# Kernel tuning notes

Measured on AMD Instinct MI355X. Metric: run time of the kernel, lower is better.

The kernel has to match this reference:

```python
import jax, jax.numpy as jnp
import numpy as np

# PDELayer config (matches torch defaults)
Nx, Ny = 48, 48
Lx, Ly = 1.0, 1.0
T, dt = 0.01, 0.001
dx, dy = Lx / Nx, Ly / Ny
Nt = int(T / dt)  # 10 sequential stencil steps
B = 16384


def setup_inputs() -> dict:
    key = jax.random.key(0)
    u0 = jax.random.normal(key, (B, 1, Nx, Ny), dtype=jnp.float32)
    alpha_w = jnp.array([0.1, 0.1, 0.1], dtype=jnp.float32)  # alpha_w1..3
    beta_w = jnp.array([0.3, 0.2, 0.2], dtype=jnp.float32)   # beta_w1..3
    return {"u0": u0, "alpha_w": alpha_w, "beta_w": beta_w}


def _coeff_grids(alpha_w, beta_w):
    x = jnp.linspace(0.0, Lx, Nx, dtype=jnp.float32)
    y = jnp.linspace(0.0, Ly, Ny, dtype=jnp.float32)
    yy, xx = jnp.meshgrid(y, x, indexing='ij')  # [Ny, Nx]
    two_pi = jnp.float32(2.0 * np.pi)
    alpha_grid = 0.5 * dt * (alpha_w[0]
                             + alpha_w[1] * jnp.sin(two_pi * yy)
                             + alpha_w[2] * jnp.sin(2.0 * two_pi * yy)) / dx ** 2
    beta_grid = dt * (beta_w[0]
                      + beta_w[1] * jnp.cos(two_pi * xx)
                      + beta_w[2] * jnp.cos(2.0 * two_pi * xx)) / dy ** 2
    return alpha_grid[None], beta_grid[None]  # [1, Nx, Ny] (Nx==Ny)


def reference(u0, alpha_w, beta_w):
    alpha_grid, beta_grid = _coeff_grids(alpha_w, beta_w)
    # reflect-pad once; boundary ring stays frozen during time stepping
    u = jnp.pad(u0[:, 0], ((0, 0), (1, 1), (1, 1)), mode='reflect')  # [B, Nx+2, Ny+2]

    def step(u, _):
        ui = u[:, 1:-1, 1:-1]
        u_xx = u[:, 2:, 1:-1] - 2.0 * ui + u[:, :-2, 1:-1]
        u_yy = u[:, 1:-1, 2:] - 2.0 * ui + u[:, 1:-1, :-2]
        u = u.at[:, 1:-1, 1:-1].set(ui + alpha_grid * u_xx + beta_grid * u_yy)
        return u, None

    u, _ = jax.lax.scan(step, u, None, length=Nt)
    return u[:, 1:-1, 1:-1][:, None]  # [B, 1, Nx, Ny]
```

## Files before the change

kernel.cpp:

```cpp
#include <hip/hip_runtime.h>


typedef float v2f __attribute__((ext_vector_type(2)));

constexpr int NXY   = 48;
constexpr int CELLS = NXY * NXY;
constexpr int NT    = 10;
constexpr int WPB   = 4;
constexpr int TPB   = 64 * WPB;

__device__ __forceinline__ float dpp_up(float oldv, float src) {
    return __int_as_float(__builtin_amdgcn_update_dpp(
        __float_as_int(oldv), __float_as_int(src), 0x111, 0xF, 0xF, false));
}
__device__ __forceinline__ float dpp_dn(float oldv, float src) {
    return __int_as_float(__builtin_amdgcn_update_dpp(
        __float_as_int(oldv), __float_as_int(src), 0x101, 0xF, 0xF, false));
}
__device__ __forceinline__ v2f dpp_up2(v2f o, v2f s) {
    v2f r; r.x = dpp_up(o.x, s.x); r.y = dpp_up(o.y, s.y); return r;
}
__device__ __forceinline__ v2f dpp_dn2(v2f o, v2f s) {
    v2f r; r.x = dpp_dn(o.x, s.x); r.y = dpp_dn(o.y, s.y); return r;
}

__global__ __launch_bounds__(TPB)
__attribute__((amdgpu_waves_per_eu(4, 8)))
void pde_heat_kernel(
    const float* __restrict__ u0,
    const float* __restrict__ aw,
    const float* __restrict__ bw,
    float* __restrict__ out)
{
    const int lane = threadIdx.x & 63;
    const int img  = blockIdx.x * WPB + (threadIdx.x >> 6);
    const int r = lane & 15;
    const int c = lane >> 4;
    const float4* __restrict__ u4 = (const float4*)(u0 + (long long)img * CELLS);
    float4*       __restrict__ o4 = (float4*)(out + (long long)img * CELLS);

    const int fb = r * 36 + c * 3;

    v2f v[3][6];
    #pragma unroll
    for (int ii = 0; ii < 3; ++ii)
        #pragma unroll
        for (int k = 0; k < 3; ++k) {
            float4 t = u4[fb + 12 * ii + k];
            v[ii][2*k]   = (v2f){t.x, t.y};
            v[ii][2*k+1] = (v2f){t.z, t.w};
        }

    const float a0 = aw[0], a1 = aw[1], a2 = aw[2];
    const float b0 = bw[0], b1 = bw[1], b2 = bw[2];
    float ca[3];
    #pragma unroll
    for (int ii = 0; ii < 3; ++ii) {
        float y = (float)(3 * r + ii) * (1.0f / 47.0f);
        ca[ii] = 1.152f * (a0 + a1 * __builtin_amdgcn_sinf(y)
                              + a2 * __builtin_amdgcn_sinf(2.0f * y));
    }
    v2f cb2[6];
    #pragma unroll
    for (int k = 0; k < 6; ++k) {
        float x0 = (float)(12 * c + 2 * k)     * (1.0f / 47.0f);
        float x1 = (float)(12 * c + 2 * k + 1) * (1.0f / 47.0f);
        cb2[k].x = 2.304f * (b0 + b1 * __builtin_amdgcn_cosf(x0)
                                + b2 * __builtin_amdgcn_cosf(2.0f * x0));
        cb2[k].y = 2.304f * (b0 + b1 * __builtin_amdgcn_cosf(x1)
                                + b2 * __builtin_amdgcn_cosf(2.0f * x1));
    }

    v2f gV[6];
    #pragma unroll
    for (int k = 0; k < 6; ++k) gV[k] = v[1][k];
    float gH[3];
    #pragma unroll
    for (int ii = 0; ii < 3; ++ii) gH[ii] = (c == 0) ? v[ii][0].y : v[ii][5].x;

    const int laneL = lane - 16, laneR = lane + 16;

    for (int t = 0; t < NT; ++t) {
        v2f hb[6], above[6];
        #pragma unroll
        for (int k = 0; k < 6; ++k) hb[k]    = dpp_dn2(gV[k], v[0][k]);
        #pragma unroll
        for (int k = 0; k < 6; ++k) above[k] = dpp_up2(gV[k], v[2][k]);

        #pragma unroll
        for (int ii = 0; ii < 3; ++ii) {
            float hl = __shfl(v[ii][5].y, laneL);
            float hr = __shfl(v[ii][0].x, laneR);
            hl = (c == 0) ? gH[ii] : hl;
            hr = (c == 3) ? gH[ii] : hr;

            v2f L[6], R[6];
            L[0] = (v2f){hl, v[ii][0].x};
            #pragma unroll
            for (int k = 1; k < 6; ++k) L[k] = (v2f){v[ii][k-1].y, v[ii][k].x};
            #pragma unroll
            for (int k = 0; k < 5; ++k) R[k] = (v2f){v[ii][k].y, v[ii][k+1].x};
            R[5] = (v2f){v[ii][5].y, hr};

            v2f nrow[6];
            #pragma unroll
            for (int k = 0; k < 6; ++k) {
                v2f cv    = v[ii][k];
                v2f below = (ii < 2) ? v[ii + 1][k] : hb[k];
                v2f uxx = (above[k] + below) - 2.0f * cv;
                v2f uyy = (L[k] + R[k])      - 2.0f * cv;
                nrow[k] = cv + ca[ii] * uxx + cb2[k] * uyy;
            }
            #pragma unroll
            for (int k = 0; k < 6; ++k) {
                above[k] = v[ii][k];
                v[ii][k] = nrow[k];
            }
        }
    }

    #pragma unroll
    for (int ii = 0; ii < 3; ++ii)
        #pragma unroll
        for (int k = 0; k < 3; ++k) {
            float4 t;
            t.x = v[ii][2*k].x;   t.y = v[ii][2*k].y;
            t.z = v[ii][2*k+1].x; t.w = v[ii][2*k+1].y;
            o4[fb + 12 * ii + k] = t;
        }
}

extern "C" void kernel_launch(void* const* d_in, const int* in_sizes, int n_in,
                              void* d_out, int out_size, void* d_ws, size_t ws_size,
                              hipStream_t stream) {
    const float* u0 = (const float*)d_in[0];
    const float* aw = (const float*)d_in[1];
    const float* bw = (const float*)d_in[2];
    float* out = (float*)d_out;

    const int B = in_sizes[0] / CELLS;
    pde_heat_kernel<<<B / WPB, TPB, 0, stream>>>(u0, aw, bw, out);
}
```

Measured before the change: 89.83 us.

## Pack two images per wavefront with six-row tiles per lane

Each wave now processes two 48x48 images, one per 32-lane half. Each lane holds a 6x12 tile instead of 3x12, which halves the thread count and the halo exchanges per cell. Vertical halos use bound-ctrl DPP row shifts with boundary selects, the time loop is fully unrolled, and the update is written as explicit fmas with per-column coefficients. The waves-per-EU hint drops to 2–4 to leave room for the larger register footprint, at the cost of less latency hiding for the global loads and stores.

```diff
diff --git a/kernel.cpp b/kernel.cpp
--- a/kernel.cpp
+++ b/kernel.cpp
@@ -9,124 +9,113 @@
 constexpr int WPB   = 4;
 constexpr int TPB   = 64 * WPB;
 
-__device__ __forceinline__ float dpp_up(float oldv, float src) {
+__device__ __forceinline__ float dpp_shr1(float x) {
     return __int_as_float(__builtin_amdgcn_update_dpp(
-        __float_as_int(oldv), __float_as_int(src), 0x111, 0xF, 0xF, false));
+        0, __float_as_int(x), 0x111, 0xF, 0xF, true));
 }
-__device__ __forceinline__ float dpp_dn(float oldv, float src) {
+__device__ __forceinline__ float dpp_shl1(float x) {
     return __int_as_float(__builtin_amdgcn_update_dpp(
-        __float_as_int(oldv), __float_as_int(src), 0x101, 0xF, 0xF, false));
-}
-__device__ __forceinline__ v2f dpp_up2(v2f o, v2f s) {
-    v2f r; r.x = dpp_up(o.x, s.x); r.y = dpp_up(o.y, s.y); return r;
-}
-__device__ __forceinline__ v2f dpp_dn2(v2f o, v2f s) {
-    v2f r; r.x = dpp_dn(o.x, s.x); r.y = dpp_dn(o.y, s.y); return r;
+        0, __float_as_int(x), 0x101, 0xF, 0xF, true));
 }
 
 __global__ __launch_bounds__(TPB)
-__attribute__((amdgpu_waves_per_eu(4, 8)))
-void pde_heat_kernel(
-    const float* __restrict__ u0,
-    const float* __restrict__ aw,
-    const float* __restrict__ bw,
-    float* __restrict__ out)
+__attribute__((amdgpu_waves_per_eu(2, 4)))
+void pde_heat_kernel(const float* __restrict__ u0,
+                     const float* __restrict__ aw,
+                     const float* __restrict__ bw,
+                     float* __restrict__ out)
 {
     const int lane = threadIdx.x & 63;
-    const int img  = blockIdx.x * WPB + (threadIdx.x >> 6);
-    const int r = lane & 15;
-    const int c = lane >> 4;
+    const int h    = lane & 31;
+    const int img  = (blockIdx.x * WPB + (threadIdx.x >> 6)) * 2 + (lane >> 5);
+    const int r = h & 7;
+    const int c = h >> 3;
+
     const float4* __restrict__ u4 = (const float4*)(u0 + (long long)img * CELLS);
     float4*       __restrict__ o4 = (float4*)(out + (long long)img * CELLS);
 
-    const int fb = r * 36 + c * 3;
-
-    v2f v[3][6];
+    v2f v[6][6];
     #pragma unroll
-    for (int ii = 0; ii < 3; ++ii)
+    for (int ii = 0; ii < 6; ++ii)
         #pragma unroll
         for (int k = 0; k < 3; ++k) {
-            float4 t = u4[fb + 12 * ii + k];
+            float4 t = u4[(r * 6 + ii) * 12 + c * 3 + k];
             v[ii][2*k]   = (v2f){t.x, t.y};
             v[ii][2*k+1] = (v2f){t.z, t.w};
         }
 
     const float a0 = aw[0], a1 = aw[1], a2 = aw[2];
     const float b0 = bw[0], b1 = bw[1], b2 = bw[2];
-    float ca[3];
+    float ca[6], cb[12];
     #pragma unroll
-    for (int ii = 0; ii < 3; ++ii) {
-        float y = (float)(3 * r + ii) * (1.0f / 47.0f);
+    for (int ii = 0; ii < 6; ++ii) {
+        float y = (float)(r * 6 + ii) * (1.0f / 47.0f);
         ca[ii] = 1.152f * (a0 + a1 * __builtin_amdgcn_sinf(y)
                               + a2 * __builtin_amdgcn_sinf(2.0f * y));
     }
-    v2f cb2[6];
     #pragma unroll
-    for (int k = 0; k < 6; ++k) {
-        float x0 = (float)(12 * c + 2 * k)     * (1.0f / 47.0f);
-        float x1 = (float)(12 * c + 2 * k + 1) * (1.0f / 47.0f);
-        cb2[k].x = 2.304f * (b0 + b1 * __builtin_amdgcn_cosf(x0)
-                                + b2 * __builtin_amdgcn_cosf(2.0f * x0));
-        cb2[k].y = 2.304f * (b0 + b1 * __builtin_amdgcn_cosf(x1)
-                                + b2 * __builtin_amdgcn_cosf(2.0f * x1));
+    for (int jj = 0; jj < 12; ++jj) {
+        float x = (float)(c * 12 + jj) * (1.0f / 47.0f);
+        cb[jj] = 2.304f * (b0 + b1 * __builtin_amdgcn_cosf(x)
+                              + b2 * __builtin_amdgcn_cosf(2.0f * x));
     }
 
     v2f gV[6];
     #pragma unroll
-    for (int k = 0; k < 6; ++k) gV[k] = v[1][k];
-    float gH[3];
+    for (int k = 0; k < 6; ++k) gV[k] = (r == 0) ? v[1][k] : v[4][k];
+    float gH[6];
     #pragma unroll
-    for (int ii = 0; ii < 3; ++ii) gH[ii] = (c == 0) ? v[ii][0].y : v[ii][5].x;
+    for (int ii = 0; ii < 6; ++ii) gH[ii] = (c == 0) ? v[ii][0].y : v[ii][5].x;
 
-    const int laneL = lane - 16, laneR = lane + 16;
+    const int laneL = lane - 8, laneR = lane + 8;
+    const bool rTop = (r == 0), rBot = (r == 7), cLft = (c == 0), cRgt = (c == 3);
 
+    #pragma unroll
     for (int t = 0; t < NT; ++t) {
-        v2f hb[6], above[6];
+        v2f ab[6], hb[6];
         #pragma unroll
-        for (int k = 0; k < 6; ++k) hb[k]    = dpp_dn2(gV[k], v[0][k]);
-        #pragma unroll
-        for (int k = 0; k < 6; ++k) above[k] = dpp_up2(gV[k], v[2][k]);
+        for (int k = 0; k < 6; ++k) {
+            float dx0 = dpp_shr1(v[5][k].x), dy0 = dpp_shr1(v[5][k].y);
+            ab[k].x = rTop ? gV[k].x : dx0;
+            ab[k].y = rTop ? gV[k].y : dy0;
+            float ex0 = dpp_shl1(v[0][k].x), ey0 = dpp_shl1(v[0][k].y);
+            hb[k].x = rBot ? gV[k].x : ex0;
+            hb[k].y = rBot ? gV[k].y : ey0;
+        }
 
         #pragma unroll
-        for (int ii = 0; ii < 3; ++ii) {
+        for (int ii = 0; ii < 6; ++ii) {
             float hl = __shfl(v[ii][5].y, laneL);
             float hr = __shfl(v[ii][0].x, laneR);
-            hl = (c == 0) ? gH[ii] : hl;
-            hr = (c == 3) ? gH[ii] : hr;
-
-            v2f L[6], R[6];
-            L[0] = (v2f){hl, v[ii][0].x};
-            #pragma unroll
-            for (int k = 1; k < 6; ++k) L[k] = (v2f){v[ii][k-1].y, v[ii][k].x};
-            #pragma unroll
-            for (int k = 0; k < 5; ++k) R[k] = (v2f){v[ii][k].y, v[ii][k+1].x};
-            R[5] = (v2f){v[ii][5].y, hr};
+            hl = cLft ? gH[ii] : hl;
+            hr = cRgt ? gH[ii] : hr;
 
             v2f nrow[6];
             #pragma unroll
             for (int k = 0; k < 6; ++k) {
                 v2f cv    = v[ii][k];
-                v2f below = (ii < 2) ? v[ii + 1][k] : hb[k];
-                v2f uxx = (above[k] + below) - 2.0f * cv;
-                v2f uyy = (L[k] + R[k])      - 2.0f * cv;
-                nrow[k] = cv + ca[ii] * uxx + cb2[k] * uyy;
+                v2f below = (ii < 5) ? v[ii + 1][k] : hb[k];
+                v2f uxx   = (ab[k] + below) - 2.0f * cv;
+                float lf0 = (k > 0) ? v[ii][k - 1].y : hl;
+                float rt1 = (k < 5) ? v[ii][k + 1].x : hr;
+                float uy0 = (lf0 + cv.y)  - 2.0f * cv.x;
+                float uy1 = (cv.x + rt1)  - 2.0f * cv.y;
+                nrow[k].x = fmaf(cb[2*k],   uy0, fmaf(ca[ii], uxx.x, cv.x));
+                nrow[k].y = fmaf(cb[2*k+1], uy1, fmaf(ca[ii], uxx.y, cv.y));
             }
             #pragma unroll
-            for (int k = 0; k < 6; ++k) {
-                above[k] = v[ii][k];
-                v[ii][k] = nrow[k];
-            }
+            for (int k = 0; k < 6; ++k) { ab[k] = v[ii][k]; v[ii][k] = nrow[k]; }
         }
     }
 
     #pragma unroll
-    for (int ii = 0; ii < 3; ++ii)
+    for (int ii = 0; ii < 6; ++ii)
         #pragma unroll
         for (int k = 0; k < 3; ++k) {
             float4 t;
             t.x = v[ii][2*k].x;   t.y = v[ii][2*k].y;
             t.z = v[ii][2*k+1].x; t.w = v[ii][2*k+1].y;
-            o4[fb + 12 * ii + k] = t;
+            o4[(r * 6 + ii) * 12 + c * 3 + k] = t;
         }
 }
 
@@ -139,5 +128,6 @@
     float* out = (float*)d_out;
 
     const int B = in_sizes[0] / CELLS;
-    pde_heat_kernel<<<B / WPB, TPB, 0, stream>>>(u0, aw, bw, out);
+    const int nBlocks = (B / 2) / WPB;
+    pde_heat_kernel<<<nBlocks, TPB, 0, stream>>>(u0, aw, bw, out);
 }
```

After: 173.6 us. 1.93x slower.
